# Kernel tuning notes

Measured on AMD Instinct MI355X. Metric: run time of the kernel, lower is better.

Reference implementation:

```python
import jax, jax.numpy as jnp
import numpy as np

B, S, D, H, DFF, L, V = 2, 512, 768, 12, 3072, 12, 32000
DK = D // H
LN_EPS = 1e-5


def setup_inputs() -> dict:
    key = jax.random.key(0)
    ks = jax.random.split(key, 24)
    s = 0.02
    n = lambda k, shp: (s * jax.random.normal(k, shp)).astype(jnp.float32)
    return dict(
        tokens=jax.random.randint(ks[0], (B, S), 0, V, dtype=jnp.int32),
        tok_emb=n(ks[1], (V, D)),
        pos_emb=n(ks[2], (S, D)),
        ln1_s=jnp.ones((L, D), jnp.float32), ln1_b=jnp.zeros((L, D), jnp.float32),
        Wq=n(ks[3], (L, D, D)), bq=jnp.zeros((L, D), jnp.float32),
        Wk=n(ks[4], (L, D, D)), bk=jnp.zeros((L, D), jnp.float32),
        Wv=n(ks[5], (L, D, D)), bv=jnp.zeros((L, D), jnp.float32),
        Wo=n(ks[6], (L, D, D)), bo=jnp.zeros((L, D), jnp.float32),
        ln2_s=jnp.ones((L, D), jnp.float32), ln2_b=jnp.zeros((L, D), jnp.float32),
        W1=n(ks[7], (L, D, DFF)), b1=jnp.zeros((L, DFF), jnp.float32),
        W2=n(ks[8], (L, DFF, D)), b2=jnp.zeros((L, D), jnp.float32),
        W_out=n(ks[9], (D, V)), b_out=jnp.zeros((V,), jnp.float32),
    )


def _layernorm(x, scale, bias):
    mu = jnp.mean(x, axis=-1, keepdims=True)
    var = jnp.mean(jnp.square(x - mu), axis=-1, keepdims=True)
    return (x - mu) * jax.lax.rsqrt(var + LN_EPS) * scale + bias


def _gpt1_forward(tokens, tok_emb, pos_emb, ln1_s, ln1_b, Wq, bq, Wk, bk, Wv, bv,
                  Wo, bo, ln2_s, ln2_b, W1, b1, W2, b2, W_out, b_out):
    b, s = tokens.shape
    x = tok_emb[tokens] + pos_emb[:s][None]  # [B,S,D]

    def step(x, p):
        (l1s, l1b, wq, bq_, wk, bk_, wv, bv_, wo, bo_, l2s, l2b, w1, b1_, w2, b2_) = p
        x2 = _layernorm(x, l1s, l1b)
        q = (x2 @ wq + bq_).reshape(b, s, H, DK)
        k = (x2 @ wk + bk_).reshape(b, s, H, DK)
        v = (x2 @ wv + bv_).reshape(b, s, H, DK)
        # NOTE: source has no causal mask (full bidirectional attention).
        scores = jnp.einsum('bqhd,bkhd->bhqk', q, k) / jnp.sqrt(jnp.float32(DK))
        attn = jax.nn.softmax(scores, axis=-1)
        ctx = jnp.einsum('bhqk,bkhd->bqhd', attn, v).reshape(b, s, D)
        x = x + ctx @ wo + bo_
        x2 = _layernorm(x, l2s, l2b)
        # torch nn.GELU default = exact (erf) GELU
        h = jax.nn.gelu(x2 @ w1 + b1_, approximate=False)
        x = x + h @ w2 + b2_
        return x, None

    params = (ln1_s, ln1_b, Wq, bq, Wk, bk, Wv, bv, Wo, bo,
              ln2_s, ln2_b, W1, b1, W2, b2)
    x, _ = jax.lax.scan(step, x, params)
    return x @ W_out + b_out  # [B,S,V]


def reference(tokens, tok_emb, pos_emb, ln1_s, ln1_b, Wq, bq, Wk, bk, Wv, bv,
              Wo, bo, ln2_s, ln2_b, W1, b1, W2, b2, W_out, b_out):
    return _gpt1_forward(tokens, tok_emb, pos_emb, ln1_s, ln1_b, Wq, bq, Wk, bk,
                         Wv, bv, Wo, bo, ln2_s, ln2_b, W1, b1, W2, b2, W_out, b_out)
```

## Files before the change

### kernel.cpp

```cpp
#include <hip/hip_runtime.h>
#include <hip/hip_bf16.h>
#include <math.h>

constexpr int BATCH = 2;
constexpr int SEQ   = 512;
constexpr int DM    = 768;
constexpr int NH    = 12;
constexpr int FF    = 3072;
constexpr int NL    = 12;
constexpr int NV    = 32000;
constexpr int HD    = 64;
constexpr int MT    = BATCH * SEQ;
constexpr int QKV   = 3 * DM;

typedef __attribute__((ext_vector_type(8))) short bf16x8;
typedef __attribute__((ext_vector_type(4))) float f32x4;

__device__ __forceinline__ float b2f(ushort u) {
    return __uint_as_float(((unsigned)u) << 16);
}
__device__ __forceinline__ ushort f2b(float f) {
    __hip_bfloat16 h = __float2bfloat16(f);
    return *reinterpret_cast<ushort*>(&h);
}

template<int N>
__device__ __forceinline__ void waitcnt_vm() {
    if constexpr (N == 0) asm volatile("s_waitcnt vmcnt(0)" ::: "memory");
    else if constexpr (N == 2) asm volatile("s_waitcnt vmcnt(2)" ::: "memory");
    else if constexpr (N == 3) asm volatile("s_waitcnt vmcnt(3)" ::: "memory");
    else if constexpr (N == 4) asm volatile("s_waitcnt vmcnt(4)" ::: "memory");
    else if constexpr (N == 6) asm volatile("s_waitcnt vmcnt(6)" ::: "memory");
    else if constexpr (N == 8) asm volatile("s_waitcnt vmcnt(8)" ::: "memory");
}

__global__ void embed_kernel(const int* __restrict__ tokens,
                             const float* __restrict__ tok_emb,
                             const float* __restrict__ pos_emb,
                             float* __restrict__ x) {
    int m = blockIdx.x;
    int s = m % SEQ;
    int t = tokens[m];
    const float* te = tok_emb + (size_t)t * DM;
    const float* pe = pos_emb + (size_t)s * DM;
    float* row = x + (size_t)m * DM;
    for (int d = threadIdx.x; d < DM; d += blockDim.x)
        row[d] = te[d] + pe[d];
}

__global__ __launch_bounds__(256) void wconv_kernel(
        const float* __restrict__ W, ushort* __restrict__ out,
        int K, int N, size_t inLS, size_t outLS, int nOff) {
    int l  = blockIdx.z;
    int n0 = blockIdx.x * 64;
    int k0 = blockIdx.y * 128;
    int tid = threadIdx.x;
    __shared__ float t[2][64][65];
    const float* src = W + (size_t)l * inLS + (size_t)k0 * N + n0;
    int r  = tid >> 4;
    int c4 = (tid & 15) * 4;
#pragma unroll
    for (int i = 0; i < 8; i++) {
        int krow = i * 16 + r;
        float4 v = *(const float4*)(src + (size_t)krow * N + c4);
        float* dstl = &t[krow >> 6][krow & 63][c4];
        dstl[0] = v.x; dstl[1] = v.y; dstl[2] = v.z; dstl[3] = v.w;
    }
    __syncthreads();
    ushort* dst = out + (size_t)l * outLS;
    int kk = (tid & 15) * 8;
    int h  = kk >> 6;
    int kb = kk & 63;
#pragma unroll
    for (int j = 0; j < 4; j++) {
        int n = j * 16 + (tid >> 4);
        ushort o[8];
#pragma unroll
        for (int m = 0; m < 8; m++) o[m] = f2b(t[h][kb + m][n]);
        *(ushort4*)(dst + (size_t)(nOff + n0 + n) * K + k0 + kk)     = *(ushort4*)&o[0];
        *(ushort4*)(dst + (size_t)(nOff + n0 + n) * K + k0 + kk + 4) = *(ushort4*)&o[4];
    }
}

__global__ void biaspack_kernel(const float* __restrict__ bq,
                                const float* __restrict__ bk,
                                const float* __restrict__ bv,
                                float* __restrict__ bqkv) {
    int idx = blockIdx.x * 256 + threadIdx.x;
    if (idx >= NL * QKV) return;
    int l = idx / QKV, c = idx % QKV;
    float v;
    if (c < DM)            v = bq[l * DM + c];
    else if (c < 2 * DM)   v = bk[l * DM + c - DM];
    else                   v = bv[l * DM + c - 2 * DM];
    bqkv[idx] = v;
}

__global__ void cvt_kernel(const float* __restrict__ in, ushort* __restrict__ out, int n) {
    int i = blockIdx.x * 256 + threadIdx.x;
    if (i < n) out[i] = f2b(in[i]);
}

__global__ __launch_bounds__(256) void ln_kernel(const float* __restrict__ x,
                                                 const float* __restrict__ sc,
                                                 const float* __restrict__ bi,
                                                 ushort* __restrict__ y) {
    int m = blockIdx.x;
    int t = threadIdx.x;
    const float* row = x + (size_t)m * DM;
    float vals[3];
    float s0 = 0.f, s1 = 0.f;
#pragma unroll
    for (int i = 0; i < 3; i++) {
        float v = row[t + 256 * i];
        vals[i] = v;
        s0 += v;
        s1 += v * v;
    }
#pragma unroll
    for (int off = 32; off >= 1; off >>= 1) {
        s0 += __shfl_down(s0, off, 64);
        s1 += __shfl_down(s1, off, 64);
    }
    __shared__ float r0[4], r1[4];
    __shared__ float mu_s, rs_s;
    int wid = t >> 6, lane = t & 63;
    if (lane == 0) { r0[wid] = s0; r1[wid] = s1; }
    __syncthreads();
    if (t == 0) {
        float a = r0[0] + r0[1] + r0[2] + r0[3];
        float q = r1[0] + r1[1] + r1[2] + r1[3];
        float mu  = a / DM;
        float var = q / DM - mu * mu;
        mu_s = mu;
        rs_s = rsqrtf(var + 1e-5f);
    }
    __syncthreads();
    float mu = mu_s, rs = rs_s;
    ushort* orow = y + (size_t)m * DM;
#pragma unroll
    for (int i = 0; i < 3; i++) {
        int d = t + 256 * i;
        orow[d] = f2b((vals[i] - mu) * rs * sc[d] + bi[d]);
    }
}

__device__ __forceinline__ void gload_lds16(const void* g, void* l) {
    __builtin_amdgcn_global_load_lds(
        (const __attribute__((address_space(1))) void*)g,
        (__attribute__((address_space(3))) void*)l, 16, 0, 0);
}

template<int BM, int BN, int WM, int WN, int NBUF, int SPLITK, int ACT,
         bool RES, bool WF32, bool WBF16, bool VT, bool ATOMIC>
__device__ __forceinline__ void gemm_body(
        const ushort* __restrict__ A, const ushort* __restrict__ BT,
        const float* __restrict__ bias, const float* __restrict__ res,
        float* __restrict__ Cf, ushort* __restrict__ Cb, ushort* __restrict__ Vt,
        int M, int N, int K) {
    constexpr int THREADS = WM * WN * 64;
    constexpr int ROWS    = BM + BN;
    constexpr int RND     = ROWS * 4 / THREADS;
    constexpr int MR      = BM / WM / 16;
    constexpr int NR      = BN / WN / 16;
    constexpr int STRIDE  = ROWS * 32;
    __shared__ ushort S_lds[NBUF * STRIDE];
    int tid = threadIdx.x;
    int il = tid & 63, wv = tid >> 6;

    int p   = blockIdx.x + gridDim.x * blockIdx.y;
    int nwg = gridDim.x * gridDim.y;
    int q8  = nwg >> 3, r8 = nwg & 7;
    int xcd = p & 7, k8 = p >> 3;
    int orig = (xcd < r8 ? xcd * (q8 + 1) : r8 * (q8 + 1) + (xcd - r8) * q8) + k8;
    int bx = orig / gridDim.y;
    int by = orig % gridDim.y;
    int bm = by * BM, bn = bx * BN;

    int kLen  = K / SPLITK;
    int kBase = blockIdx.z * kLen;

    const ushort* src[RND];
    int dstOff[RND];
#pragma unroll
    for (int r = 0; r < RND; r++) {
        int f = r * THREADS + tid;
        int row = f >> 2, seg = f & 3;
        int lseg = seg ^ ((row >> 1) & 3);
        src[r] = (row < BM ? A + (size_t)(bm + row) * K
                           : BT + (size_t)(bn + row - BM) * K) + kBase + lseg * 8;
        dstOff[r] = (r * THREADS + wv * 64) * 8;
    }

    int wm = wv / WN, wn = wv % WN;
    int lr = il & 15;
    int lkS = ((il >> 4) ^ ((lr >> 1) & 3)) * 8;
    f32x4 acc[MR][NR] = {};

    int nt = kLen >> 5;

#pragma unroll
    for (int b = 0; b < NBUF - 1; b++)
#pragma unroll
        for (int r = 0; r < RND; r++)
            gload_lds16(src[r] + b * 32, &S_lds[b * STRIDE + dstOff[r]]);
    waitcnt_vm<RND * (NBUF - 2)>();
    __builtin_amdgcn_s_barrier();

    int cur = 0;
    for (int t = 0; t < nt; ++t) {
        if (t + NBUF - 1 < nt) {
            int sb = cur + NBUF - 1; if (sb >= NBUF) sb -= NBUF;
            int kofs = (t + NBUF - 1) * 32;
            ushort* Bp = &S_lds[sb * STRIDE];
#pragma unroll
            for (int r = 0; r < RND; r++) gload_lds16(src[r] + kofs, &Bp[dstOff[r]]);
        }

        const ushort* base = &S_lds[cur * STRIDE];
        bf16x8 af[MR], bfr[NR];
#pragma unroll
        for (int i = 0; i < MR; i++)
            af[i] = *(const bf16x8*)&base[(wm * (BM / WM) + i * 16 + lr) * 32 + lkS];
#pragma unroll
        for (int i = 0; i < NR; i++)
            bfr[i] = *(const bf16x8*)&base[(BM + wn * (BN / WN) + i * 16 + lr) * 32 + lkS];
        __builtin_amdgcn_s_setprio(1);
#pragma unroll
        for (int mi = 0; mi < MR; mi++)
#pragma unroll
            for (int ni = 0; ni < NR; ni++)
                acc[mi][ni] = __builtin_amdgcn_mfma_f32_16x16x32_bf16(
                    af[mi], bfr[ni], acc[mi][ni], 0, 0, 0);
        __builtin_amdgcn_s_setprio(0);

        if (t + 1 < nt) {
            int k = nt - t - 2;
            if (k > NBUF - 2) k = NBUF - 2;
            switch (k) {
                case 0:  waitcnt_vm<0>(); break;
                case 1:  waitcnt_vm<RND>(); break;
                default: waitcnt_vm<2 * RND>(); break;
            }
            __builtin_amdgcn_s_barrier();
        }
        cur = (cur + 1 == NBUF) ? 0 : cur + 1;
    }

    bool addBias = bias && (SPLITK == 1 || blockIdx.z == 0);
#pragma unroll
    for (int mi = 0; mi < MR; mi++) {
        int row0 = bm + wm * (BM / WM) + mi * 16 + (il >> 4) * 4;
#pragma unroll
        for (int ni = 0; ni < NR; ni++) {
            int col = bn + wn * (BN / WN) + ni * 16 + (il & 15);
            float bv = addBias ? bias[col] : 0.f;
#pragma unroll
            for (int j = 0; j < 4; j++) {
                int r = row0 + j;
                float v = acc[mi][ni][j] + bv;
                if (ACT == 1) v = 0.5f * v * (1.0f + erff(v * 0.70710678118654752f));
                if (RES) v += res[(size_t)r * N + col];
                if (ATOMIC) atomicAdd(&Cf[(size_t)r * N + col], v);
                else if (WF32) Cf[(size_t)r * N + col] = v;
                if (WBF16) {
                    if (VT && bn >= 2 * DM) {
                        int d  = col - 2 * DM;
                        int hh = d >> 6, dd = d & 63;
                        int bb = r >> 9, s = r & (SEQ - 1);
                        Vt[((size_t)(bb * NH + hh) * HD + dd) * SEQ + s] = f2b(v);
                    } else {
                        Cb[(size_t)r * N + col] = f2b(v);
                    }
                }
            }
        }
    }
}

__global__ __launch_bounds__(256) void gemm_qkv(
        const ushort* A, const ushort* BT, const float* bias,
        ushort* Cb, ushort* Vt, int M, int N, int K) {
    gemm_body<64, 128, 2, 2, 4, 1, 0, false, false, true, true, false>(
        A, BT, bias, nullptr, nullptr, Cb, Vt, M, N, K);
}
__global__ __launch_bounds__(256) void gemm_wo(
        const ushort* A, const ushort* BT, const float* bias,
        float* Cf, int M, int N, int K) {
    gemm_body<64, 64, 2, 2, 4, 2, 0, false, false, false, false, true>(
        A, BT, bias, nullptr, Cf, nullptr, nullptr, M, N, K);
}
__global__ __launch_bounds__(256) void gemm_w1(
        const ushort* A, const ushort* BT, const float* bias,
        ushort* Cb, int M, int N, int K) {
    gemm_body<64, 128, 2, 2, 4, 1, 1, false, false, true, false, false>(
        A, BT, bias, nullptr, nullptr, Cb, nullptr, M, N, K);
}
__global__ __launch_bounds__(256) void gemm_w2(
        const ushort* A, const ushort* BT, const float* bias,
        float* Cf, int M, int N, int K) {
    gemm_body<64, 64, 2, 2, 4, 2, 0, false, false, false, false, true>(
        A, BT, bias, nullptr, Cf, nullptr, nullptr, M, N, K);
}
__global__ __launch_bounds__(512) void gemm_logits(
        const ushort* A, const ushort* BT, const float* bias,
        float* Cf, int M, int N, int K) {
    gemm_body<256, 256, 2, 4, 4, 1, 0, false, true, false, false, false>(
        A, BT, bias, nullptr, Cf, nullptr, nullptr, M, N, K);
}

__device__ __forceinline__ char* swzp(void* base, int row, int colByte) {
    return (char*)base + ((row * 128 + colByte) ^ ((row & 7) << 4));
}
__device__ __forceinline__ const char* swzpc(const void* base, int row, int colByte) {
    return (const char*)base + ((row * 128 + colByte) ^ ((row & 7) << 4));
}

__global__ __launch_bounds__(256) void fattn_kernel(
        const ushort* __restrict__ qkv, const ushort* __restrict__ vt,
        ushort* __restrict__ ctx) {
    int qt = blockIdx.x;
    int h  = blockIdx.y;
    int b  = blockIdx.z;
    int tid = threadIdx.x;
    int il = tid & 63, wv = tid >> 6;
    int qsub = wv & 1, grp = wv >> 1;

    __shared__ __align__(16) char smem[41 * 1024];
    ushort* Ks = (ushort*)(smem + grp * 8192);
    ushort* Vs = (ushort*)(smem + 16384 + grp * 8192);
    ushort* Ps = (ushort*)(smem + 32768 + wv * 2048);
    float*  Om = (float*)smem;
    float*  Ss = (float*)(smem + 16384);

    int bh = b * NH + h;
    const ushort* kbase = qkv + (size_t)b * SEQ * QKV + DM + h * HD;
    const ushort* vbase = vt + (size_t)bh * HD * SEQ;

    int lr = il & 15, lg = il >> 4;
    int qrow = qt * 32 + qsub * 16 + lr;
    const ushort* qptr = qkv + (size_t)(b * SEQ + qrow) * QKV + h * HD + lg * 8;
    bf16x8 qf0 = *(const bf16x8*)qptr;
    bf16x8 qf1 = *(const bf16x8*)(qptr + 32);

    f32x4 accO[4] = {};
    float sm[4] = {0.f, 0.f, 0.f, 0.f};

    int lig  = qsub * 64 + il;
    int srow = lig >> 3;
    int sseg = (lig & 7) * 8;

    for (int kt = 0; kt < 4; kt++) {
        int k0 = grp * 256 + kt * 64;
        bf16x8 kreg[4], vreg[4];
#pragma unroll
        for (int r = 0; r < 4; r++) {
            int row = r * 16 + srow;
            kreg[r] = *(const bf16x8*)(kbase + (size_t)(k0 + row) * QKV + sseg);
            vreg[r] = *(const bf16x8*)(vbase + (size_t)row * SEQ + k0 + sseg);
        }
        __syncthreads();
#pragma unroll
        for (int r = 0; r < 4; r++) {
            int row = r * 16 + srow;
            *(bf16x8*)swzp(Ks, row, sseg * 2) = kreg[r];
            *(bf16x8*)swzp(Vs, row, sseg * 2) = vreg[r];
        }
        __syncthreads();

        f32x4 accS[4] = {};
        __builtin_amdgcn_s_setprio(1);
#pragma unroll
        for (int nf = 0; nf < 4; nf++) {
            bf16x8 b0 = *(const bf16x8*)swzpc(Ks, nf * 16 + lr, lg * 16);
            bf16x8 b1 = *(const bf16x8*)swzpc(Ks, nf * 16 + lr, 64 + lg * 16);
            accS[nf] = __builtin_amdgcn_mfma_f32_16x16x32_bf16(qf0, b0, accS[nf], 0, 0, 0);
            accS[nf] = __builtin_amdgcn_mfma_f32_16x16x32_bf16(qf1, b1, accS[nf], 0, 0, 0);
        }
        __builtin_amdgcn_s_setprio(0);

        float pv[4][4];
#pragma unroll
        for (int nf = 0; nf < 4; nf++)
#pragma unroll
            for (int j = 0; j < 4; j++)
                pv[nf][j] = __expf(fmaf(accS[nf][j], 0.125f, -8.0f));
#pragma unroll
        for (int j = 0; j < 4; j++) {
            float rs = (pv[0][j] + pv[1][j]) + (pv[2][j] + pv[3][j]);
            rs += __shfl_xor(rs, 1, 64);
            rs += __shfl_xor(rs, 2, 64);
            rs += __shfl_xor(rs, 4, 64);
            rs += __shfl_xor(rs, 8, 64);
            sm[j] += rs;
        }

#pragma unroll
        for (int nf = 0; nf < 4; nf++)
#pragma unroll
            for (int j = 0; j < 4; j++)
                *(ushort*)swzp(Ps, lg * 4 + j, (nf * 16 + lr) * 2) = f2b(pv[nf][j]);

        bf16x8 pa0 = *(const bf16x8*)swzpc(Ps, lr, lg * 16);
        bf16x8 pa1 = *(const bf16x8*)swzpc(Ps, lr, 64 + lg * 16);
        __builtin_amdgcn_s_setprio(1);
#pragma unroll
        for (int nf = 0; nf < 4; nf++) {
            bf16x8 v0 = *(const bf16x8*)swzpc(Vs, nf * 16 + lr, lg * 16);
            bf16x8 v1 = *(const bf16x8*)swzpc(Vs, nf * 16 + lr, 64 + lg * 16);
            accO[nf] = __builtin_amdgcn_mfma_f32_16x16x32_bf16(pa0, v0, accO[nf], 0, 0, 0);
            accO[nf] = __builtin_amdgcn_mfma_f32_16x16x32_bf16(pa1, v1, accO[nf], 0, 0, 0);
        }
        __builtin_amdgcn_s_setprio(0);
    }

    __syncthreads();
    if (grp == 1) {
#pragma unroll
        for (int nf = 0; nf < 4; nf++)
#pragma unroll
            for (int j = 0; j < 4; j++)
                Om[(qsub * 16 + lg * 4 + j) * 64 + nf * 16 + lr] = accO[nf][j];
        if (lr == 0) {
#pragma unroll
            for (int j = 0; j < 4; j++)
                Ss[qsub * 16 + lg * 4 + j] = sm[j];
        }
    }
    __syncthreads();
    if (grp == 0) {
        ushort* obase = ctx + (size_t)(b * SEQ + qt * 32 + qsub * 16) * DM + h * HD;
#pragma unroll
        for (int j = 0; j < 4; j++) {
            int q = lg * 4 + j;
            float inv = 1.0f / (sm[j] + Ss[qsub * 16 + q]);
#pragma unroll
            for (int nf = 0; nf < 4; nf++) {
                int d = nf * 16 + lr;
                float o1 = Om[(qsub * 16 + q) * 64 + d];
                obase[(size_t)q * DM + d] = f2b((accO[nf][j] + o1) * inv);
            }
        }
    }
}

extern "C" void kernel_launch(void* const* d_in, const int* in_sizes, int n_in,
                              void* d_out, int out_size, void* d_ws, size_t ws_size,
                              hipStream_t stream) {
    const int*   tokens  = (const int*)d_in[0];
    const float* tok_emb = (const float*)d_in[1];
    const float* pos_emb = (const float*)d_in[2];
    const float* ln1_s   = (const float*)d_in[3];
    const float* ln1_b   = (const float*)d_in[4];
    const float* Wq      = (const float*)d_in[5];
    const float* bq      = (const float*)d_in[6];
    const float* Wk      = (const float*)d_in[7];
    const float* bk      = (const float*)d_in[8];
    const float* Wv      = (const float*)d_in[9];
    const float* bv      = (const float*)d_in[10];
    const float* Wo      = (const float*)d_in[11];
    const float* bo      = (const float*)d_in[12];
    const float* ln2_s   = (const float*)d_in[13];
    const float* ln2_b   = (const float*)d_in[14];
    const float* W1      = (const float*)d_in[15];
    const float* b1      = (const float*)d_in[16];
    const float* W2      = (const float*)d_in[17];
    const float* b2      = (const float*)d_in[18];
    const float* W_out   = (const float*)d_in[19];
    const float* b_out   = (const float*)d_in[20];

    char* ws = (char*)d_ws;
    size_t off = 0;
    auto alloc = [&](size_t bytes) { size_t o = off; off = (off + bytes + 255) & ~(size_t)255; return o; };

    float*  x    = (float*)(ws + alloc((size_t)MT * DM * 4));
    ushort* x2b  = (ushort*)(ws + alloc((size_t)MT * DM * 2));
    ushort* qkvb = (ushort*)(ws + alloc((size_t)MT * QKV * 2));
    ushort* cb   = (ushort*)(ws + alloc((size_t)MT * DM * 2));
    ushort* hb   = (ushort*)(ws + alloc((size_t)MT * FF * 2));
    ushort* xb   = (ushort*)(ws + alloc((size_t)MT * DM * 2));
    ushort* vtb  = (ushort*)(ws + alloc((size_t)BATCH * NH * HD * SEQ * 2));
    float*  bqkv = (float*)(ws + alloc((size_t)NL * QKV * 4));

    size_t szQkvT = (size_t)NL * QKV * DM;
    size_t szWoT  = (size_t)NL * DM * DM;
    size_t szW1T  = (size_t)NL * FF * DM;
    size_t szW2T  = (size_t)NL * DM * FF;
    size_t szWoutT= (size_t)NV * DM;

    size_t actEnd = off;
    size_t fullNeed = actEnd + 2 * (szQkvT + szWoT + szW1T + szW2T + szWoutT) + 5 * 256;
    bool full = (fullNeed <= ws_size);

    ushort *WqkvT, *WoT, *W1T, *W2T, *WoutT;
    if (full) {
        WqkvT = (ushort*)(ws + alloc(szQkvT * 2));
        WoT   = (ushort*)(ws + alloc(szWoT * 2));
        W1T   = (ushort*)(ws + alloc(szW1T * 2));
        W2T   = (ushort*)(ws + alloc(szW2T * 2));
        WoutT = (ushort*)(ws + alloc(szWoutT * 2));
    } else {
        size_t layerElems = (size_t)QKV * DM + (size_t)DM * DM + 2 * (size_t)FF * DM;
        size_t regionElems = layerElems > szWoutT ? layerElems : szWoutT;
        ushort* region = (ushort*)(ws + alloc(regionElems * 2));
        WqkvT = region;
        WoT   = WqkvT + (size_t)QKV * DM;
        W1T   = WoT + (size_t)DM * DM;
        W2T   = W1T + (size_t)FF * DM;
        WoutT = region;
    }

    biaspack_kernel<<<(NL * QKV + 255) / 256, 256, 0, stream>>>(bq, bk, bv, bqkv);
    embed_kernel<<<MT, 256, 0, stream>>>(tokens, tok_emb, pos_emb, x);

    if (full) {
        dim3 gD(DM / 64, DM / 128, NL);
        wconv_kernel<<<gD, 256, 0, stream>>>(Wq, WqkvT, DM, DM, (size_t)DM * DM, (size_t)QKV * DM, 0);
        wconv_kernel<<<gD, 256, 0, stream>>>(Wk, WqkvT, DM, DM, (size_t)DM * DM, (size_t)QKV * DM, DM);
        wconv_kernel<<<gD, 256, 0, stream>>>(Wv, WqkvT, DM, DM, (size_t)DM * DM, (size_t)QKV * DM, 2 * DM);
        wconv_kernel<<<gD, 256, 0, stream>>>(Wo, WoT, DM, DM, (size_t)DM * DM, (size_t)DM * DM, 0);
        dim3 g1(FF / 64, DM / 128, NL);
        wconv_kernel<<<g1, 256, 0, stream>>>(W1, W1T, DM, FF, (size_t)DM * FF, (size_t)FF * DM, 0);
        dim3 g2(DM / 64, FF / 128, NL);
        wconv_kernel<<<g2, 256, 0, stream>>>(W2, W2T, FF, DM, (size_t)FF * DM, (size_t)DM * FF, 0);
        dim3 go(NV / 64, DM / 128, 1);
        wconv_kernel<<<go, 256, 0, stream>>>(W_out, WoutT, DM, NV, 0, 0, 0);
    }

    for (int l = 0; l < NL; l++) {
        ushort* wqkv = WqkvT + (full ? (size_t)l * QKV * DM : 0);
        ushort* wo   = WoT   + (full ? (size_t)l * DM * DM  : 0);
        ushort* w1   = W1T   + (full ? (size_t)l * FF * DM  : 0);
        ushort* w2   = W2T   + (full ? (size_t)l * DM * FF  : 0);
        if (!full) {
            dim3 gD(DM / 64, DM / 128, 1);
            wconv_kernel<<<gD, 256, 0, stream>>>(Wq + (size_t)l * DM * DM, wqkv, DM, DM, 0, 0, 0);
            wconv_kernel<<<gD, 256, 0, stream>>>(Wk + (size_t)l * DM * DM, wqkv, DM, DM, 0, 0, DM);
            wconv_kernel<<<gD, 256, 0, stream>>>(Wv + (size_t)l * DM * DM, wqkv, DM, DM, 0, 0, 2 * DM);
            wconv_kernel<<<gD, 256, 0, stream>>>(Wo + (size_t)l * DM * DM, wo, DM, DM, 0, 0, 0);
            dim3 g1(FF / 64, DM / 128, 1);
            wconv_kernel<<<g1, 256, 0, stream>>>(W1 + (size_t)l * DM * FF, w1, DM, FF, 0, 0, 0);
            dim3 g2(DM / 64, FF / 128, 1);
            wconv_kernel<<<g2, 256, 0, stream>>>(W2 + (size_t)l * FF * DM, w2, FF, DM, 0, 0, 0);
        }

        ln_kernel<<<MT, 256, 0, stream>>>(x, ln1_s + l * DM, ln1_b + l * DM, x2b);

        gemm_qkv<<<dim3(QKV / 128, MT / 64), 256, 0, stream>>>(
            x2b, wqkv, bqkv + (size_t)l * QKV, qkvb, vtb, MT, QKV, DM);

        fattn_kernel<<<dim3(SEQ / 32, NH, BATCH), 256, 0, stream>>>(qkvb, vtb, cb);

        gemm_wo<<<dim3(DM / 64, MT / 64, 2), 256, 0, stream>>>(
            cb, wo, bo + (size_t)l * DM, x, MT, DM, DM);

        ln_kernel<<<MT, 256, 0, stream>>>(x, ln2_s + l * DM, ln2_b + l * DM, x2b);

        gemm_w1<<<dim3(FF / 128, MT / 64), 256, 0, stream>>>(
            x2b, w1, b1 + (size_t)l * FF, hb, MT, FF, DM);

        gemm_w2<<<dim3(DM / 64, MT / 64, 2), 256, 0, stream>>>(
            hb, w2, b2 + (size_t)l * DM, x, MT, DM, FF);
    }

    if (!full) {
        dim3 go(NV / 64, DM / 128, 1);
        wconv_kernel<<<go, 256, 0, stream>>>(W_out, WoutT, DM, NV, 0, 0, 0);
    }
    cvt_kernel<<<(MT * DM + 255) / 256, 256, 0, stream>>>(x, xb, MT * DM);

    gemm_logits<<<dim3(NV / 256, MT / 256), 512, 0, stream>>>(
        xb, WoutT, b_out, (float*)d_out, MT, NV, DM);
}
```

Baseline: 1.271 ms.

## Load K/V MFMA fragments directly from global and remap attention blocks per XCD

The attention kernel no longer stages K and V tiles through shared memory with two barriers per tile. Each wave now loads its MFMA B-operand fragments straight from global memory into registers. This shrinks LDS use from 41KB to about 8KB and removes the per-tile __syncthreads. The grid becomes 1D and is remapped so that consecutive blocks on the same XCD share a head and batch, which should improve L2 reuse of K/V. In exchange, each wave issues more redundant global loads, since the two q-subtile waves fetch the same K/V rows, and those accesses are less coalesced.

```diff
diff --git a/kernel.cpp b/kernel.cpp
--- a/kernel.cpp
+++ b/kernel.cpp
@@ -319,23 +319,24 @@
 __global__ __launch_bounds__(256) void fattn_kernel(
         const ushort* __restrict__ qkv, const ushort* __restrict__ vt,
         ushort* __restrict__ ctx) {
-    int qt = blockIdx.x;
-    int h  = blockIdx.y;
-    int b  = blockIdx.z;
+    int p = blockIdx.x;
+    int nwg = gridDim.x;
+    int orig = (p & 7) * (nwg >> 3) + (p >> 3);
+    int qt = orig & 15;
+    int hb = orig >> 4;
+    int h = hb % NH, b = hb / NH;
+
     int tid = threadIdx.x;
     int il = tid & 63, wv = tid >> 6;
     int qsub = wv & 1, grp = wv >> 1;
 
-    __shared__ __align__(16) char smem[41 * 1024];
-    ushort* Ks = (ushort*)(smem + grp * 8192);
-    ushort* Vs = (ushort*)(smem + 16384 + grp * 8192);
-    ushort* Ps = (ushort*)(smem + 32768 + wv * 2048);
+    __shared__ __align__(16) char smem[8448];
+    ushort* Ps = (ushort*)(smem + wv * 2048);
     float*  Om = (float*)smem;
-    float*  Ss = (float*)(smem + 16384);
-
-    int bh = b * NH + h;
+    float*  Ss = (float*)(smem + 8192);
+
     const ushort* kbase = qkv + (size_t)b * SEQ * QKV + DM + h * HD;
-    const ushort* vbase = vt + (size_t)bh * HD * SEQ;
+    const ushort* vbase = vt + (size_t)hb * HD * SEQ;
 
     int lr = il & 15, lg = il >> 4;
     int qrow = qt * 32 + qsub * 16 + lr;
@@ -346,38 +347,33 @@
     f32x4 accO[4] = {};
     float sm[4] = {0.f, 0.f, 0.f, 0.f};
 
-    int lig  = qsub * 64 + il;
-    int srow = lig >> 3;
-    int sseg = (lig & 7) * 8;
-
     for (int kt = 0; kt < 4; kt++) {
         int k0 = grp * 256 + kt * 64;
-        bf16x8 kreg[4], vreg[4];
-#pragma unroll
-        for (int r = 0; r < 4; r++) {
-            int row = r * 16 + srow;
-            kreg[r] = *(const bf16x8*)(kbase + (size_t)(k0 + row) * QKV + sseg);
-            vreg[r] = *(const bf16x8*)(vbase + (size_t)row * SEQ + k0 + sseg);
-        }
-        __syncthreads();
-#pragma unroll
-        for (int r = 0; r < 4; r++) {
-            int row = r * 16 + srow;
-            *(bf16x8*)swzp(Ks, row, sseg * 2) = kreg[r];
-            *(bf16x8*)swzp(Vs, row, sseg * 2) = vreg[r];
-        }
-        __syncthreads();
+
+        bf16x8 kb0[4], kb1[4];
+#pragma unroll
+        for (int nf = 0; nf < 4; nf++) {
+            const ushort* kr = kbase + (size_t)(k0 + nf * 16 + lr) * QKV + lg * 8;
+            kb0[nf] = *(const bf16x8*)kr;
+            kb1[nf] = *(const bf16x8*)(kr + 32);
+        }
 
         f32x4 accS[4] = {};
         __builtin_amdgcn_s_setprio(1);
 #pragma unroll
         for (int nf = 0; nf < 4; nf++) {
-            bf16x8 b0 = *(const bf16x8*)swzpc(Ks, nf * 16 + lr, lg * 16);
-            bf16x8 b1 = *(const bf16x8*)swzpc(Ks, nf * 16 + lr, 64 + lg * 16);
-            accS[nf] = __builtin_amdgcn_mfma_f32_16x16x32_bf16(qf0, b0, accS[nf], 0, 0, 0);
-            accS[nf] = __builtin_amdgcn_mfma_f32_16x16x32_bf16(qf1, b1, accS[nf], 0, 0, 0);
+            accS[nf] = __builtin_amdgcn_mfma_f32_16x16x32_bf16(qf0, kb0[nf], accS[nf], 0, 0, 0);
+            accS[nf] = __builtin_amdgcn_mfma_f32_16x16x32_bf16(qf1, kb1[nf], accS[nf], 0, 0, 0);
         }
         __builtin_amdgcn_s_setprio(0);
+
+        bf16x8 vb0[4], vb1[4];
+#pragma unroll
+        for (int nf = 0; nf < 4; nf++) {
+            const ushort* vr = vbase + (size_t)(nf * 16 + lr) * SEQ + k0 + lg * 8;
+            vb0[nf] = *(const bf16x8*)vr;
+            vb1[nf] = *(const bf16x8*)(vr + 32);
+        }
 
         float pv[4][4];
 #pragma unroll
@@ -406,10 +402,8 @@
         __builtin_amdgcn_s_setprio(1);
 #pragma unroll
         for (int nf = 0; nf < 4; nf++) {
-            bf16x8 v0 = *(const bf16x8*)swzpc(Vs, nf * 16 + lr, lg * 16);
-            bf16x8 v1 = *(const bf16x8*)swzpc(Vs, nf * 16 + lr, 64 + lg * 16);
-            accO[nf] = __builtin_amdgcn_mfma_f32_16x16x32_bf16(pa0, v0, accO[nf], 0, 0, 0);
-            accO[nf] = __builtin_amdgcn_mfma_f32_16x16x32_bf16(pa1, v1, accO[nf], 0, 0, 0);
+            accO[nf] = __builtin_amdgcn_mfma_f32_16x16x32_bf16(pa0, vb0[nf], accO[nf], 0, 0, 0);
+            accO[nf] = __builtin_amdgcn_mfma_f32_16x16x32_bf16(pa1, vb1[nf], accO[nf], 0, 0, 0);
         }
         __builtin_amdgcn_s_setprio(0);
     }
@@ -549,7 +543,7 @@
         gemm_qkv<<<dim3(QKV / 128, MT / 64), 256, 0, stream>>>(
             x2b, wqkv, bqkv + (size_t)l * QKV, qkvb, vtb, MT, QKV, DM);
 
-        fattn_kernel<<<dim3(SEQ / 32, NH, BATCH), 256, 0, stream>>>(qkvb, vtb, cb);
+        fattn_kernel<<<SEQ / 32 * NH * BATCH, 256, 0, stream>>>(qkvb, vtb, cb);
 
         gemm_wo<<<dim3(DM / 64, MT / 64, 2), 256, 0, stream>>>(
             cb, wo, bo + (size_t)l * DM, x, MT, DM, DM);
```

Measured after the change: 1.361 ms. 1.07x slower.
